# Kernel optimization log

Hardware: AMD Instinct MI355X
Metric: run time of the kernel (lower is better)

Reference implementation:

```python
import jax, jax.numpy as jnp
import numpy as np

B, S, D = 2, 2048, 1024
H, DK = 16, 64            # n_heads, d_k = d_model // n_heads
EXP = 4                   # pattern-separation expand_factor
ED = DK * EXP             # expanded_dim = 256
TOPK = 32                 # top-k kept after ReLU expansion
ALPHA = 0.05
TNT = 1.0                 # trace_norm_target


def setup_inputs() -> dict:
    key = jax.random.key(0)
    ks = jax.random.split(key, 8)
    sc = 1.0 / np.sqrt(D)
    x = jax.random.normal(ks[0], (B, S, D), jnp.float32)
    W_q = jax.random.normal(ks[1], (D, D), jnp.float32) * sc
    W_k = jax.random.normal(ks[2], (D, D), jnp.float32) * sc
    W_v = jax.random.normal(ks[3], (D, D), jnp.float32) * sc
    W_o = jax.random.normal(ks[4], (D, D), jnp.float32) * sc
    # trace buffers (non-zero so the trace read path actually matters)
    traces = jax.random.normal(ks[5], (H, DK, DK), jnp.float32) * 0.02
    value_traces = jax.random.normal(ks[6], (H, ED, DK), jnp.float32) * 0.02
    # frozen random expansion projection (dentate gyrus), W / sqrt(d_k)
    W_expand = jax.random.normal(ks[7], (DK, ED), jnp.float32) / np.sqrt(DK)
    return dict(x=x, W_q=W_q, W_k=W_k, W_v=W_v, W_o=W_o,
                traces=traces, value_traces=value_traces, W_expand=W_expand)


def _eff_alpha(T):
    # alpha / (1 + ||T_h||_F / trace_norm_target), shape (1, H, 1, 1)
    norms = jnp.sqrt(jnp.sum(T * T, axis=(1, 2)))
    return (ALPHA / (1.0 + norms / TNT)).reshape(1, -1, 1, 1)


def _forward(x, W_q, W_k, W_v, W_o, traces, value_traces, W_expand):
    b, s, d = x.shape
    def proj(W):
        return jnp.einsum('bsd,de->bse', x, W).reshape(b, s, H, DK).transpose(0, 2, 1, 3)
    Q, K, V = proj(W_q), proj(W_k), proj(W_v)  # (B, H, S, DK)

    scores = jnp.einsum('bhqd,bhkd->bhqk', Q, K)
    # score trace bias: alpha_eff * (Q @ T @ K^T)
    QT = jnp.einsum('bhqd,hde->bhqe', Q, traces)
    trace_scores = jnp.einsum('bhqe,bhke->bhqk', QT, K)
    scores = (scores + _eff_alpha(traces) * trace_scores) / np.sqrt(DK)
    A = jax.nn.softmax(scores, axis=-1)
    out = jnp.einsum('bhqk,bhkd->bhqd', A, V)

    # value trace read with use_key_q shift: address with previous token's Q
    Q_addr = jnp.concatenate([jnp.zeros_like(Q[:, :, :1, :]), Q[:, :, :-1, :]], axis=2)
    # pattern separation: frozen random expansion + ReLU + top-k sparsify
    Q_exp = jax.nn.relu(jnp.einsum('bhsd,de->bhse', Q_addr, W_expand))  # (B,H,S,ED)
    kth = jax.lax.top_k(Q_exp, TOPK)[0][..., -1:]
    Q_sparse = jnp.where(Q_exp >= kth, Q_exp, 0.0)  # == scatter of top-k vals (ties at 0 contribute 0)
    stored = jnp.einsum('bhse,hed->bhsd', Q_sparse, value_traces)
    out = out + _eff_alpha(value_traces) * stored

    out = out.transpose(0, 2, 1, 3).reshape(b, s, d)
    return jnp.einsum('bsd,de->bse', out, W_o)


def reference(x, W_q, W_k, W_v, W_o, traces, value_traces, W_expand):
    return _forward(x, W_q, W_k, W_v, W_o, traces, value_traces, W_expand)
```

## Files before the change

### kernel.cpp

```cpp
#include <hip/hip_runtime.h>
#include <stdint.h>

#define Bn 2
#define Sn 2048
#define Dn 1024
#define Hn 16
#define DKn 64
#define EDn 256

typedef __attribute__((ext_vector_type(8))) short bvec8;
typedef __attribute__((ext_vector_type(4))) float fvec4;

#define MFMA(a, b, c) __builtin_amdgcn_mfma_f32_16x16x32_bf16(a, b, c, 0, 0, 0)

__device__ __forceinline__ float b2f(unsigned short u) {
  return __uint_as_float(((unsigned)u) << 16);
}
__device__ __forceinline__ unsigned short f2b(float x) {
  unsigned u = __float_as_uint(x);
  u += 0x7fffu + ((u >> 16) & 1u);
  return (unsigned short)(u >> 16);
}
__device__ __forceinline__ unsigned pk2(float a, float b) {
  return ((__float_as_uint(a) + 0x8000u) >> 16) |
         ((__float_as_uint(b) + 0x8000u) & 0xffff0000u);
}
__device__ __forceinline__ void g2l(const unsigned short* g, unsigned short* l) {
  __builtin_amdgcn_global_load_lds(
      (const __attribute__((address_space(1))) void*)g,
      (__attribute__((address_space(3))) void*)l, 16, 0, 0);
}

__global__ __launch_bounds__(256) void k_prep1(
    const float* __restrict__ x, const float* __restrict__ w0,
    const float* __restrict__ w1, const float* __restrict__ w2,
    const float* __restrict__ w3, const float* __restrict__ traces,
    const float* __restrict__ vtr, const float* __restrict__ Wexp,
    unsigned short* __restrict__ Wt, unsigned short* __restrict__ WexpT,
    unsigned short* __restrict__ xb, float* __restrict__ alphas,
    unsigned short* __restrict__ VTt) {
  const int blk = blockIdx.x;
  const int tid = threadIdx.x;
  __shared__ unsigned short Tl[64][72];
  if (blk < 1024) {
    int z = blk >> 8, t = blk & 255;
    int n0 = (t & 15) * 64, k0 = (t >> 4) * 64;
    const float* src = (z == 0) ? w0 : ((z == 1) ? w1 : ((z == 2) ? w2 : w3));
    unsigned short* d = Wt + (size_t)z * Dn * Dn;
#pragma unroll
    for (int i = 0; i < 4; ++i) {
      int q = tid + 256 * i;
      int kr = q >> 4, c4 = q & 15;
      float4 v = *(const float4*)&src[(size_t)(k0 + kr) * Dn + n0 + 4 * c4];
      ushort4 u;
      u.x = f2b(v.x); u.y = f2b(v.y); u.z = f2b(v.z); u.w = f2b(v.w);
      *(ushort4*)&Tl[kr][4 * c4] = u;
    }
    __syncthreads();
#pragma unroll
    for (int i = 0; i < 4; ++i) {
      int q = tid + 256 * i;
      int nr = q >> 4, c4 = q & 15;
      ushort4 u;
      u.x = Tl[4 * c4 + 0][nr]; u.y = Tl[4 * c4 + 1][nr];
      u.z = Tl[4 * c4 + 2][nr]; u.w = Tl[4 * c4 + 3][nr];
      *(ushort4*)&d[(size_t)(n0 + nr) * Dn + k0 + 4 * c4] = u;
    }
  } else if (blk < 1028) {
    int e0 = (blk - 1024) * 64;
#pragma unroll
    for (int i = 0; i < 4; ++i) {
      int q = tid + 256 * i;
      int dr = q >> 4, c4 = q & 15;
      float4 v = *(const float4*)&Wexp[(size_t)dr * EDn + e0 + 4 * c4];
      ushort4 u;
      u.x = f2b(v.x); u.y = f2b(v.y); u.z = f2b(v.z); u.w = f2b(v.w);
      *(ushort4*)&Tl[dr][4 * c4] = u;
    }
    __syncthreads();
#pragma unroll
    for (int i = 0; i < 4; ++i) {
      int q = tid + 256 * i;
      int er = q >> 4, c4 = q & 15;
      ushort4 u;
      u.x = Tl[4 * c4 + 0][er]; u.y = Tl[4 * c4 + 1][er];
      u.z = Tl[4 * c4 + 2][er]; u.w = Tl[4 * c4 + 3][er];
      *(ushort4*)&WexpT[(size_t)(e0 + er) * DKn + 4 * c4] = u;
    }
  } else if (blk < 5124) {
    size_t i = ((size_t)(blk - 1028) * 256 + tid) * 4;
    float4 v = *(const float4*)&x[i];
    ushort4 u;
    u.x = f2b(v.x); u.y = f2b(v.y); u.z = f2b(v.z); u.w = f2b(v.w);
    *(ushort4*)&xb[i] = u;
  } else if (blk < 5156) {
    int a = blk - 5124;
    const float* base;
    int n;
    if (a < 16) { base = traces + a * DKn * DKn; n = DKn * DKn; }
    else        { base = vtr + (a - 16) * EDn * DKn; n = EDn * DKn; }
    float s = 0.f;
    for (int i = tid; i < n; i += 256) { float v = base[i]; s += v * v; }
    __shared__ float red[256];
    red[tid] = s;
    __syncthreads();
    for (int off = 128; off > 0; off >>= 1) {
      if (tid < off) red[tid] += red[tid + off];
      __syncthreads();
    }
    if (tid == 0) alphas[a] = 0.05f / (1.f + sqrtf(red[0]));
  } else {
    int t = blk - 5156;
    int e0 = (t & 3) * 64, h = t >> 2;
    const float* src = vtr + (size_t)h * EDn * DKn;
    unsigned short* dst = VTt + (size_t)h * DKn * EDn;
#pragma unroll
    for (int i = 0; i < 4; ++i) {
      int q = tid + 256 * i;
      int er = q >> 4, c4 = q & 15;
      float4 v = *(const float4*)&src[(size_t)(e0 + er) * DKn + 4 * c4];
      ushort4 u;
      u.x = f2b(v.x); u.y = f2b(v.y); u.z = f2b(v.z); u.w = f2b(v.w);
      *(ushort4*)&Tl[er][4 * c4] = u;
    }
    __syncthreads();
#pragma unroll
    for (int i = 0; i < 4; ++i) {
      int q = tid + 256 * i;
      int dr = q >> 4, c4 = q & 15;
      ushort4 u;
      u.x = Tl[4 * c4 + 0][dr]; u.y = Tl[4 * c4 + 1][dr];
      u.z = Tl[4 * c4 + 2][dr]; u.w = Tl[4 * c4 + 3][dr];
      *(ushort4*)&dst[(size_t)dr * EDn + e0 + 4 * c4] = u;
    }
  }
}

__global__ __launch_bounds__(256) void k_mkM(const float* __restrict__ tr,
                                             const float* __restrict__ alph,
                                             unsigned short* __restrict__ Mt) {
  const float SC = 0.125f * 1.4426950408889634f;
  int h = blockIdx.x;
  float a = alph[h] * SC;
  const float* th = tr + (size_t)h * DKn * DKn;
  unsigned short* mh = Mt + (size_t)h * DKn * DKn;
  for (int i = threadIdx.x; i < DKn * DKn; i += 256) {
    int e = i >> 6, k = i & 63;
    float v = a * th[(size_t)k * DKn + e] + ((e == k) ? SC : 0.f);
    mh[i] = f2b(v);
  }
}

template <int MODE>
__global__ __launch_bounds__(256) void k_gemm(
    const unsigned short* __restrict__ Ab,
    const unsigned short* __restrict__ BtBase, unsigned short* __restrict__ Qb,
    unsigned short* __restrict__ Kb, unsigned short* __restrict__ VtOut,
    float* __restrict__ Cout) {
  const int z = (MODE == 0) ? blockIdx.z : 0;
  const unsigned short* Bt = BtBase + (size_t)z * Dn * Dn;
  __shared__ unsigned short As[128 * 32];
  __shared__ unsigned short Bs[128 * 32];
  const int tid = threadIdx.x;
  const int w = tid >> 6, lane = tid & 63, qd = lane >> 4, cc = lane & 15;
  const int m0 = blockIdx.y * 128, n0 = blockIdx.x * 128;
  const int mW = 64 * (w >> 1), nW = 64 * (w & 1);
  const int srow = lane >> 2;
  const int schk = 8 * ((lane & 3) ^ (srow & 3));
  const int r0 = 32 * w + srow, r1 = r0 + 16;
  const bool swap = (MODE == 1) || (z != 2);
  fvec4 acc[4][4];
#pragma unroll
  for (int i = 0; i < 4; ++i)
#pragma unroll
    for (int j = 0; j < 4; ++j) acc[i][j] = (fvec4){0.f, 0.f, 0.f, 0.f};

  for (int k0 = 0; k0 < Dn; k0 += 32) {
    g2l(&Ab[(size_t)(m0 + r0) * Dn + k0 + schk], &As[1024 * w]);
    g2l(&Ab[(size_t)(m0 + r1) * Dn + k0 + schk], &As[1024 * w + 512]);
    g2l(&Bt[(size_t)(n0 + r0) * Dn + k0 + schk], &Bs[1024 * w]);
    g2l(&Bt[(size_t)(n0 + r1) * Dn + k0 + schk], &Bs[1024 * w + 512]);
    __syncthreads();
    bvec8 af[4], bf[4];
#pragma unroll
    for (int i = 0; i < 4; ++i) {
      int ra = mW + 16 * i + cc;
      af[i] = *(const bvec8*)&As[ra * 32 + 8 * (qd ^ (ra & 3))];
      int rb = nW + 16 * i + cc;
      bf[i] = *(const bvec8*)&Bs[rb * 32 + 8 * (qd ^ (rb & 3))];
    }
    if (swap) {
#pragma unroll
      for (int i = 0; i < 4; ++i)
#pragma unroll
        for (int j = 0; j < 4; ++j) acc[i][j] = MFMA(bf[j], af[i], acc[i][j]);
    } else {
#pragma unroll
      for (int i = 0; i < 4; ++i)
#pragma unroll
        for (int j = 0; j < 4; ++j) acc[i][j] = MFMA(af[i], bf[j], acc[i][j]);
    }
    __syncthreads();
  }
#pragma unroll
  for (int i = 0; i < 4; ++i)
#pragma unroll
    for (int j = 0; j < 4; ++j) {
      if (MODE == 1) {
        int s = m0 + mW + 16 * i + cc;
        int nb = n0 + nW + 16 * j + 4 * qd;
        float4 v = make_float4(acc[i][j][0], acc[i][j][1], acc[i][j][2],
                               acc[i][j][3]);
        *(float4*)&Cout[(size_t)s * Dn + nb] = v;
      } else if (z == 2) {
        int rowb = m0 + mW + 16 * i + 4 * qd;
        int col = n0 + nW + 16 * j + cc;
        int b = rowb >> 11, s = rowb & 2047;
        int h = col >> 6, dk = col & 63;
        ushort4 u;
        u.x = f2b(acc[i][j][0]); u.y = f2b(acc[i][j][1]);
        u.z = f2b(acc[i][j][2]); u.w = f2b(acc[i][j][3]);
        *(ushort4*)&VtOut[(((size_t)(b * Hn + h)) * DKn + dk) * Sn + s] = u;
      } else {
        int s = m0 + mW + 16 * i + cc;
        int col = n0 + nW + 16 * j + 4 * qd;
        int b = s >> 11;
        int sm = s & 2047;
        int h = col >> 6, dk = col & 63;
        unsigned short* Cb = (z == 0) ? Qb : Kb;
        ushort4 u;
        u.x = f2b(acc[i][j][0]); u.y = f2b(acc[i][j][1]);
        u.z = f2b(acc[i][j][2]); u.w = f2b(acc[i][j][3]);
        *(ushort4*)&Cb[(((size_t)(b * Hn + h)) * Sn + sm) * DKn + dk] = u;
      }
    }
}

__global__ __launch_bounds__(256, 2) void k_pattsep(
    const unsigned short* __restrict__ Qb,
    const unsigned short* __restrict__ WexpT,
    const unsigned short* __restrict__ VTt,
    const float* __restrict__ alphas, unsigned short* __restrict__ ATb) {
  __shared__ uint4 Wl4[2048];
  __shared__ uint4 Vl4[2048];
  __shared__ uint4 Ps4[4][256];
  const int tile = blockIdx.x, bh = blockIdx.y;
  const int b = bh >> 4, h = bh & 15;
  const int tid = threadIdx.x;
  const int w = tid >> 6, lane = tid & 63, qd = lane >> 4, cc = lane & 15;
  const float avt = alphas[16 + h];

  const uint4* wsrc = (const uint4*)WexpT;
  const uint4* vsrc = (const uint4*)(VTt + (size_t)h * DKn * EDn);
  for (int i = tid; i < 2048; i += 256) {
    int e = i >> 3, c = i & 7;
    Wl4[e * 8 + (c ^ (e & 7))] = wsrc[i];
    int d = i >> 5, c2 = i & 31;
    Vl4[d * 32 + (c2 ^ (d & 7))] = vsrc[i];
  }
  __syncthreads();

  const unsigned short* Wls = (const unsigned short*)Wl4;
  const unsigned short* Vls = (const unsigned short*)Vl4;
  unsigned short* Pw = (unsigned short*)Ps4[w];

  for (int rg = 0; rg < 2; ++rg) {
    const int s0 = tile * 128 + w * 32 + rg * 16;
    bvec8 aq0 = {}, aq1 = {};
    const int srow = s0 + cc;
    if (srow > 0) {
      const unsigned short* qp = Qb + ((size_t)bh * Sn + srow - 1) * DKn;
      aq0 = *(const bvec8*)&qp[8 * qd];
      aq1 = *(const bvec8*)&qp[32 + 8 * qd];
    }
    fvec4 E[16];
#pragma unroll
    for (int j = 0; j < 16; ++j) {
      const int e = 16 * j + cc;
      const unsigned short* wr = Wls + e * 64;
      bvec8 b0 = *(const bvec8*)&wr[8 * (qd ^ (e & 7))];
      bvec8 b1 = *(const bvec8*)&wr[8 * ((4 + qd) ^ (e & 7))];
      fvec4 zv = {0.f, 0.f, 0.f, 0.f};
      zv = MFMA(aq0, b0, zv);
      E[j] = MFMA(aq1, b1, zv);
    }
#pragma unroll
    for (int j = 0; j < 16; ++j)
#pragma unroll
      for (int r = 0; r < 4; ++r) E[j][r] = fmaxf(E[j][r], 0.f);

    float thr[4];
#pragma unroll
    for (int r = 0; r < 4; ++r) {
      unsigned cur = 0u;
      bool done = false;
      for (int bit = 30; bit >= 0; --bit) {
        unsigned cand = cur | (1u << bit);
        float t = __uint_as_float(cand);
        int cnt = 0;
#pragma unroll
        for (int j = 0; j < 16; ++j) cnt += (E[j][r] >= t) ? 1 : 0;
        cnt += __shfl_xor(cnt, 1);
        cnt += __shfl_xor(cnt, 2);
        cnt += __shfl_xor(cnt, 4);
        cnt += __shfl_xor(cnt, 8);
        if (!done && cnt >= 32) {
          cur = cand;
          if (cnt == 32) done = true;
        }
        if (__all(done)) break;
      }
      thr[r] = __uint_as_float(cur);
    }

    fvec4 acc2[4];
#pragma unroll
    for (int j2 = 0; j2 < 4; ++j2) acc2[j2] = (fvec4){0.f, 0.f, 0.f, 0.f};

#pragma unroll
    for (int half = 0; half < 2; ++half) {
#pragma unroll
      for (int j = 0; j < 8; ++j) {
        const int jj = j + 8 * half;
#pragma unroll
        for (int r = 0; r < 4; ++r) {
          float v = E[jj][r];
          bool sel = (v >= thr[r]) && (v > 0.f);
          int row = 4 * qd + r;
          int s = 16 * j + cc;
          int ch = (s >> 3) ^ (row & 7);
          Pw[row * 128 + ch * 8 + (s & 7)] = sel ? f2b(v) : (unsigned short)0;
        }
      }
#pragma unroll
      for (int j2 = 0; j2 < 4; ++j2) {
        const int d = 16 * j2 + cc;
        const unsigned short* vr = Vls + d * 256;
#pragma unroll
        for (int c = 0; c < 4; ++c) {
          int cg = 4 * (c + 4 * half) + qd;
          bvec8 bv = *(const bvec8*)&vr[8 * (cg ^ (d & 7))];
          int ca = 4 * c + qd;
          bvec8 ap = *(const bvec8*)&Pw[cc * 128 + 8 * (ca ^ (cc & 7))];
          acc2[j2] = MFMA(ap, bv, acc2[j2]);
        }
      }
    }
#pragma unroll
    for (int j2 = 0; j2 < 4; ++j2)
#pragma unroll
      for (int r = 0; r < 4; ++r) {
        int row = s0 + 4 * qd + r;
        ATb[((size_t)(b * Sn + row)) * Dn + h * DKn + 16 * j2 + cc] =
            f2b(avt * acc2[j2][r]);
      }
  }
}

__global__ __launch_bounds__(256) void k_attn(
    const unsigned short* __restrict__ Qb, const unsigned short* __restrict__ Kb,
    const unsigned short* __restrict__ Vt, const unsigned short* __restrict__ Mt,
    unsigned short* __restrict__ ATb) {
  __shared__ unsigned short Kd[64 * 64];
  __shared__ unsigned short Vl[64 * 64];
  __shared__ unsigned short Ps[4][16][72];
  const int bh = blockIdx.x, qt = blockIdx.y;
  const int b = bh >> 4, h = bh & 15;
  const int tid = threadIdx.x;
  const int w = tid >> 6, lane = tid & 63, qd = lane >> 4, cc = lane & 15;

  const unsigned short* qg = Qb + ((size_t)bh * Sn + qt * 64 + w * 16) * DKn;
  bvec8 a0 = *(const bvec8*)&qg[cc * DKn + 8 * qd];
  bvec8 a1 = *(const bvec8*)&qg[cc * DKn + 32 + 8 * qd];
  const unsigned short* mh = Mt + (size_t)h * DKn * DKn;
#pragma unroll
  for (int j = 0; j < 4; ++j) {
    bvec8 b0 = *(const bvec8*)&mh[(size_t)(16 * j + cc) * DKn + 8 * qd];
    bvec8 b1 = *(const bvec8*)&mh[(size_t)(16 * j + cc) * DKn + 32 + 8 * qd];
    fvec4 zz = {0.f, 0.f, 0.f, 0.f};
    zz = MFMA(a0, b0, zz);
    zz = MFMA(a1, b1, zz);
#pragma unroll
    for (int r = 0; r < 4; ++r) {
      int qr = 4 * qd + r;
      Kd[(16 * w + qr) * 64 + 8 * ((2 * j + (cc >> 3)) ^ (qr & 7)) + (cc & 7)] =
          f2b(zz[r]);
    }
  }
  bvec8 aq0 = *(const bvec8*)&Kd[(16 * w + cc) * 64 + 8 * (qd ^ (cc & 7))];
  bvec8 aq1 =
      *(const bvec8*)&Kd[(16 * w + cc) * 64 + 8 * ((qd + 4) ^ (cc & 7))];

  float l_s = 0.f;
  fvec4 O[4];
#pragma unroll
  for (int j = 0; j < 4; ++j) O[j] = (fvec4){0.f, 0.f, 0.f, 0.f};

  const int vrow = lane >> 3;
  const int vchk = 8 * ((lane & 7) ^ (vrow & 7));
  const unsigned short* kgb = Kb + (size_t)bh * Sn * DKn;
  const unsigned short* vgb = Vt + (size_t)bh * DKn * Sn;

  for (int kt = 0; kt < Sn / 64; ++kt) {
    __syncthreads();
    const unsigned short* kg = kgb + (size_t)kt * 64 * DKn;
    g2l(&kg[(size_t)(16 * w + vrow) * 64 + vchk], &Kd[1024 * w]);
    g2l(&kg[(size_t)(16 * w + 8 + vrow) * 64 + vchk], &Kd[1024 * w + 512]);
    g2l(&vgb[(size_t)(16 * w + vrow) * Sn + kt * 64 + vchk], &Vl[1024 * w]);
    g2l(&vgb[(size_t)(16 * w + 8 + vrow) * Sn + kt * 64 + vchk],
        &Vl[1024 * w + 512]);
    __syncthreads();
    fvec4 sc[4];
#pragma unroll
    for (int j = 0; j < 4; ++j) {
      int rk = 16 * j + cc;
      bvec8 b0 = *(const bvec8*)&Kd[rk * 64 + 8 * (qd ^ (cc & 7))];
      bvec8 b1 = *(const bvec8*)&Kd[rk * 64 + 8 * ((qd + 4) ^ (cc & 7))];
      fvec4 zz = {0.f, 0.f, 0.f, 0.f};
      zz = MFMA(b0, aq0, zz);
      sc[j] = MFMA(b1, aq1, zz);
    }
#pragma unroll
    for (int j = 0; j < 4; ++j) {
      float p0 = __builtin_amdgcn_exp2f(sc[j][0]);
      float p1 = __builtin_amdgcn_exp2f(sc[j][1]);
      float p2 = __builtin_amdgcn_exp2f(sc[j][2]);
      float p3 = __builtin_amdgcn_exp2f(sc[j][3]);
      l_s += (p0 + p1) + (p2 + p3);
      uint2 u;
      u.x = pk2(p0, p1);
      u.y = pk2(p2, p3);
      *(uint2*)&Ps[w][cc][16 * j + 4 * qd] = u;
    }
    bvec8 ap0 = *(const bvec8*)&Ps[w][cc][8 * qd];
    bvec8 ap1 = *(const bvec8*)&Ps[w][cc][32 + 8 * qd];
#pragma unroll
    for (int j = 0; j < 4; ++j) {
      int rv = 16 * j + cc;
      bvec8 v0 = *(const bvec8*)&Vl[rv * 64 + 8 * (qd ^ (cc & 7))];
      bvec8 v1 = *(const bvec8*)&Vl[rv * 64 + 8 * ((qd + 4) ^ (cc & 7))];
      O[j] = MFMA(ap0, v0, O[j]);
      O[j] = MFMA(ap1, v1, O[j]);
    }
  }
  l_s += __shfl_xor(l_s, 16);
  l_s += __shfl_xor(l_s, 32);
  float linv = 1.f / l_s;
  float inv[4];
#pragma unroll
  for (int r = 0; r < 4; ++r) inv[r] = __shfl(linv, 4 * qd + r);
#pragma unroll
  for (int j = 0; j < 4; ++j)
#pragma unroll
    for (int r = 0; r < 4; ++r) {
      int row = qt * 64 + w * 16 + 4 * qd + r;
      unsigned short* p =
          ATb + ((size_t)(b * Sn + row)) * Dn + h * DKn + 16 * j + cc;
      *p = f2b(b2f(*p) + O[j][r] * inv[r]);
    }
}

extern "C" void kernel_launch(void* const* d_in, const int* in_sizes, int n_in,
                              void* d_out, int out_size, void* d_ws,
                              size_t ws_size, hipStream_t stream) {
  const float* x = (const float*)d_in[0];
  const float* Wq = (const float*)d_in[1];
  const float* Wk = (const float*)d_in[2];
  const float* Wv = (const float*)d_in[3];
  const float* Wo = (const float*)d_in[4];
  const float* traces = (const float*)d_in[5];
  const float* vtr = (const float*)d_in[6];
  const float* Wexp = (const float*)d_in[7];

  const size_t NQ = (size_t)Bn * Hn * Sn * DKn;
  unsigned short* Qb = (unsigned short*)d_ws;
  unsigned short* Kb = Qb + NQ;
  unsigned short* Vt = Kb + NQ;
  unsigned short* Wt = Vt + NQ;
  unsigned short* Mt = Wt + NQ;
  unsigned short* WexpT = Mt + 65536;
  unsigned short* VTt = WexpT + 16384;
  float* alph = (float*)(VTt + 262144);
  unsigned short* ATb = (unsigned short*)(alph + 32);
  unsigned short* xb = ATb;

  k_prep1<<<5220, 256, 0, stream>>>(x, Wq, Wk, Wv, Wo, traces, vtr, Wexp, Wt,
                                    WexpT, xb, alph, VTt);
  k_mkM<<<16, 256, 0, stream>>>(traces, alph, Mt);
  k_gemm<0><<<dim3(8, 32, 3), 256, 0, stream>>>(xb, Wt, Qb, Kb, Vt, nullptr);
  k_pattsep<<<dim3(16, 32), 256, 0, stream>>>(Qb, WexpT, VTt, alph, ATb);
  k_attn<<<dim3(32, 32), 256, 0, stream>>>(Qb, Kb, Vt, Mt, ATb);
  k_gemm<1><<<dim3(8, 32, 1), 256, 0, stream>>>(
      ATb, Wt + 3 * (size_t)Dn * Dn, nullptr, nullptr, nullptr,
      (float*)d_out);
}
```

Before: 315.4 us.

## Process two key tiles per barrier in attention and fold M build into prep

The attention loop now stages 128 keys and values per iteration in two LDS buffers. This halves the number of block-wide barriers and gives more global-to-LDS loads in flight per sync. The P scratch uses an XOR-swizzled 64-wide layout to reduce bank conflicts. Separately, the trace-norm and M-matrix construction move into the prep kernel, removing one launch and its serial dependency. The trade-off is a larger LDS footprint per attention block, which may lower how many blocks fit per CU.

```diff
diff --git a/kernel.cpp b/kernel.cpp
--- a/kernel.cpp
+++ b/kernel.cpp
@@ -31,19 +31,102 @@
       (__attribute__((address_space(3))) void*)l, 16, 0, 0);
 }
 
-__global__ __launch_bounds__(256) void k_prep1(
+__global__ __launch_bounds__(256) void k_prep(
     const float* __restrict__ x, const float* __restrict__ w0,
     const float* __restrict__ w1, const float* __restrict__ w2,
     const float* __restrict__ w3, const float* __restrict__ traces,
     const float* __restrict__ vtr, const float* __restrict__ Wexp,
     unsigned short* __restrict__ Wt, unsigned short* __restrict__ WexpT,
     unsigned short* __restrict__ xb, float* __restrict__ alphas,
-    unsigned short* __restrict__ VTt) {
+    unsigned short* __restrict__ VTt, unsigned short* __restrict__ Mt) {
   const int blk = blockIdx.x;
   const int tid = threadIdx.x;
   __shared__ unsigned short Tl[64][72];
-  if (blk < 1024) {
-    int z = blk >> 8, t = blk & 255;
+  __shared__ float red[256];
+  if (blk < 16) {
+    const float* base = vtr + (size_t)blk * EDn * DKn;
+    float s = 0.f;
+    for (int i = tid; i < EDn * DKn; i += 256) { float v = base[i]; s += v * v; }
+    red[tid] = s;
+    __syncthreads();
+    for (int off = 128; off > 0; off >>= 1) {
+      if (tid < off) red[tid] += red[tid + off];
+      __syncthreads();
+    }
+    if (tid == 0) alphas[16 + blk] = 0.05f / (1.f + sqrtf(red[0]));
+  } else if (blk < 32) {
+    __shared__ float Ts[DKn * DKn];
+    const float SC = 0.125f * 1.4426950408889634f;
+    int h = blk - 16;
+    const float* th = traces + (size_t)h * DKn * DKn;
+    float s = 0.f;
+    for (int i = tid; i < DKn * DKn; i += 256) {
+      float v = th[i];
+      Ts[i] = v;
+      s += v * v;
+    }
+    red[tid] = s;
+    __syncthreads();
+    for (int off = 128; off > 0; off >>= 1) {
+      if (tid < off) red[tid] += red[tid + off];
+      __syncthreads();
+    }
+    float a = (0.05f / (1.f + sqrtf(red[0]))) * SC;
+    unsigned short* mh = Mt + (size_t)h * DKn * DKn;
+    for (int i = tid; i < DKn * DKn; i += 256) {
+      int e = i >> 6, k = i & 63;
+      float v = a * Ts[k * DKn + e] + ((e == k) ? SC : 0.f);
+      mh[i] = f2b(v);
+    }
+  } else if (blk < 96) {
+    int t = blk - 32;
+    int e0 = (t & 3) * 64, h = t >> 2;
+    const float* src = vtr + (size_t)h * EDn * DKn;
+    unsigned short* dst = VTt + (size_t)h * DKn * EDn;
+#pragma unroll
+    for (int i = 0; i < 4; ++i) {
+      int q = tid + 256 * i;
+      int er = q >> 4, c4 = q & 15;
+      float4 v = *(const float4*)&src[(size_t)(e0 + er) * DKn + 4 * c4];
+      ushort4 u;
+      u.x = f2b(v.x); u.y = f2b(v.y); u.z = f2b(v.z); u.w = f2b(v.w);
+      *(ushort4*)&Tl[er][4 * c4] = u;
+    }
+    __syncthreads();
+#pragma unroll
+    for (int i = 0; i < 4; ++i) {
+      int q = tid + 256 * i;
+      int dr = q >> 4, c4 = q & 15;
+      ushort4 u;
+      u.x = Tl[4 * c4 + 0][dr]; u.y = Tl[4 * c4 + 1][dr];
+      u.z = Tl[4 * c4 + 2][dr]; u.w = Tl[4 * c4 + 3][dr];
+      *(ushort4*)&dst[(size_t)dr * EDn + e0 + 4 * c4] = u;
+    }
+  } else if (blk < 100) {
+    int e0 = (blk - 96) * 64;
+#pragma unroll
+    for (int i = 0; i < 4; ++i) {
+      int q = tid + 256 * i;
+      int dr = q >> 4, c4 = q & 15;
+      float4 v = *(const float4*)&Wexp[(size_t)dr * EDn + e0 + 4 * c4];
+      ushort4 u;
+      u.x = f2b(v.x); u.y = f2b(v.y); u.z = f2b(v.z); u.w = f2b(v.w);
+      *(ushort4*)&Tl[dr][4 * c4] = u;
+    }
+    __syncthreads();
+#pragma unroll
+    for (int i = 0; i < 4; ++i) {
+      int q = tid + 256 * i;
+      int er = q >> 4, c4 = q & 15;
+      ushort4 u;
+      u.x = Tl[4 * c4 + 0][er]; u.y = Tl[4 * c4 + 1][er];
+      u.z = Tl[4 * c4 + 2][er]; u.w = Tl[4 * c4 + 3][er];
+      *(ushort4*)&WexpT[(size_t)(e0 + er) * DKn + 4 * c4] = u;
+    }
+  } else if (blk < 1124) {
+    int t = blk - 100;
+    int z = t >> 8;
+    t &= 255;
     int n0 = (t & 15) * 64, k0 = (t >> 4) * 64;
     const float* src = (z == 0) ? w0 : ((z == 1) ? w1 : ((z == 2) ? w2 : w3));
     unsigned short* d = Wt + (size_t)z * Dn * Dn;
@@ -66,88 +149,12 @@
       u.z = Tl[4 * c4 + 2][nr]; u.w = Tl[4 * c4 + 3][nr];
       *(ushort4*)&d[(size_t)(n0 + nr) * Dn + k0 + 4 * c4] = u;
     }
-  } else if (blk < 1028) {
-    int e0 = (blk - 1024) * 64;
-#pragma unroll
-    for (int i = 0; i < 4; ++i) {
-      int q = tid + 256 * i;
-      int dr = q >> 4, c4 = q & 15;
-      float4 v = *(const float4*)&Wexp[(size_t)dr * EDn + e0 + 4 * c4];
-      ushort4 u;
-      u.x = f2b(v.x); u.y = f2b(v.y); u.z = f2b(v.z); u.w = f2b(v.w);
-      *(ushort4*)&Tl[dr][4 * c4] = u;
-    }
-    __syncthreads();
-#pragma unroll
-    for (int i = 0; i < 4; ++i) {
-      int q = tid + 256 * i;
-      int er = q >> 4, c4 = q & 15;
-      ushort4 u;
-      u.x = Tl[4 * c4 + 0][er]; u.y = Tl[4 * c4 + 1][er];
-      u.z = Tl[4 * c4 + 2][er]; u.w = Tl[4 * c4 + 3][er];
-      *(ushort4*)&WexpT[(size_t)(e0 + er) * DKn + 4 * c4] = u;
-    }
-  } else if (blk < 5124) {
-    size_t i = ((size_t)(blk - 1028) * 256 + tid) * 4;
+  } else {
+    size_t i = ((size_t)(blk - 1124) * 256 + tid) * 4;
     float4 v = *(const float4*)&x[i];
     ushort4 u;
     u.x = f2b(v.x); u.y = f2b(v.y); u.z = f2b(v.z); u.w = f2b(v.w);
     *(ushort4*)&xb[i] = u;
-  } else if (blk < 5156) {
-    int a = blk - 5124;
-    const float* base;
-    int n;
-    if (a < 16) { base = traces + a * DKn * DKn; n = DKn * DKn; }
-    else        { base = vtr + (a - 16) * EDn * DKn; n = EDn * DKn; }
-    float s = 0.f;
-    for (int i = tid; i < n; i += 256) { float v = base[i]; s += v * v; }
-    __shared__ float red[256];
-    red[tid] = s;
-    __syncthreads();
-    for (int off = 128; off > 0; off >>= 1) {
-      if (tid < off) red[tid] += red[tid + off];
-      __syncthreads();
-    }
-    if (tid == 0) alphas[a] = 0.05f / (1.f + sqrtf(red[0]));
-  } else {
-    int t = blk - 5156;
-    int e0 = (t & 3) * 64, h = t >> 2;
-    const float* src = vtr + (size_t)h * EDn * DKn;
-    unsigned short* dst = VTt + (size_t)h * DKn * EDn;
-#pragma unroll
-    for (int i = 0; i < 4; ++i) {
-      int q = tid + 256 * i;
-      int er = q >> 4, c4 = q & 15;
-      float4 v = *(const float4*)&src[(size_t)(e0 + er) * DKn + 4 * c4];
-      ushort4 u;
-      u.x = f2b(v.x); u.y = f2b(v.y); u.z = f2b(v.z); u.w = f2b(v.w);
-      *(ushort4*)&Tl[er][4 * c4] = u;
-    }
-    __syncthreads();
-#pragma unroll
-    for (int i = 0; i < 4; ++i) {
-      int q = tid + 256 * i;
-      int dr = q >> 4, c4 = q & 15;
-      ushort4 u;
-      u.x = Tl[4 * c4 + 0][dr]; u.y = Tl[4 * c4 + 1][dr];
-      u.z = Tl[4 * c4 + 2][dr]; u.w = Tl[4 * c4 + 3][dr];
-      *(ushort4*)&dst[(size_t)dr * EDn + e0 + 4 * c4] = u;
-    }
-  }
-}
-
-__global__ __launch_bounds__(256) void k_mkM(const float* __restrict__ tr,
-                                             const float* __restrict__ alph,
-                                             unsigned short* __restrict__ Mt) {
-  const float SC = 0.125f * 1.4426950408889634f;
-  int h = blockIdx.x;
-  float a = alph[h] * SC;
-  const float* th = tr + (size_t)h * DKn * DKn;
-  unsigned short* mh = Mt + (size_t)h * DKn * DKn;
-  for (int i = threadIdx.x; i < DKn * DKn; i += 256) {
-    int e = i >> 6, k = i & 63;
-    float v = a * th[(size_t)k * DKn + e] + ((e == k) ? SC : 0.f);
-    mh[i] = f2b(v);
   }
 }
 
@@ -361,9 +368,9 @@
     const unsigned short* __restrict__ Qb, const unsigned short* __restrict__ Kb,
     const unsigned short* __restrict__ Vt, const unsigned short* __restrict__ Mt,
     unsigned short* __restrict__ ATb) {
-  __shared__ unsigned short Kd[64 * 64];
-  __shared__ unsigned short Vl[64 * 64];
-  __shared__ unsigned short Ps[4][16][72];
+  __shared__ unsigned short Kd2[2][4096];
+  __shared__ unsigned short Vl2[2][4096];
+  __shared__ unsigned short Ps[4][2048];
   const int bh = blockIdx.x, qt = blockIdx.y;
   const int b = bh >> 4, h = bh & 15;
   const int tid = threadIdx.x;
@@ -383,13 +390,13 @@
 #pragma unroll
     for (int r = 0; r < 4; ++r) {
       int qr = 4 * qd + r;
-      Kd[(16 * w + qr) * 64 + 8 * ((2 * j + (cc >> 3)) ^ (qr & 7)) + (cc & 7)] =
-          f2b(zz[r]);
+      Kd2[0][(16 * w + qr) * 64 + 8 * ((2 * j + (cc >> 3)) ^ (qr & 7)) +
+             (cc & 7)] = f2b(zz[r]);
     }
   }
-  bvec8 aq0 = *(const bvec8*)&Kd[(16 * w + cc) * 64 + 8 * (qd ^ (cc & 7))];
+  bvec8 aq0 = *(const bvec8*)&Kd2[0][(16 * w + cc) * 64 + 8 * (qd ^ (cc & 7))];
   bvec8 aq1 =
-      *(const bvec8*)&Kd[(16 * w + cc) * 64 + 8 * ((qd + 4) ^ (cc & 7))];
+      *(const bvec8*)&Kd2[0][(16 * w + cc) * 64 + 8 * ((qd + 4) ^ (cc & 7))];
 
   float l_s = 0.f;
   fvec4 O[4];
@@ -400,47 +407,61 @@
   const int vchk = 8 * ((lane & 7) ^ (vrow & 7));
   const unsigned short* kgb = Kb + (size_t)bh * Sn * DKn;
   const unsigned short* vgb = Vt + (size_t)bh * DKn * Sn;
-
-  for (int kt = 0; kt < Sn / 64; ++kt) {
-    __syncthreads();
-    const unsigned short* kg = kgb + (size_t)kt * 64 * DKn;
-    g2l(&kg[(size_t)(16 * w + vrow) * 64 + vchk], &Kd[1024 * w]);
-    g2l(&kg[(size_t)(16 * w + 8 + vrow) * 64 + vchk], &Kd[1024 * w + 512]);
-    g2l(&vgb[(size_t)(16 * w + vrow) * Sn + kt * 64 + vchk], &Vl[1024 * w]);
-    g2l(&vgb[(size_t)(16 * w + 8 + vrow) * Sn + kt * 64 + vchk],
-        &Vl[1024 * w + 512]);
-    __syncthreads();
-    fvec4 sc[4];
-#pragma unroll
-    for (int j = 0; j < 4; ++j) {
-      int rk = 16 * j + cc;
-      bvec8 b0 = *(const bvec8*)&Kd[rk * 64 + 8 * (qd ^ (cc & 7))];
-      bvec8 b1 = *(const bvec8*)&Kd[rk * 64 + 8 * ((qd + 4) ^ (cc & 7))];
-      fvec4 zz = {0.f, 0.f, 0.f, 0.f};
-      zz = MFMA(b0, aq0, zz);
-      sc[j] = MFMA(b1, aq1, zz);
-    }
-#pragma unroll
-    for (int j = 0; j < 4; ++j) {
-      float p0 = __builtin_amdgcn_exp2f(sc[j][0]);
-      float p1 = __builtin_amdgcn_exp2f(sc[j][1]);
-      float p2 = __builtin_amdgcn_exp2f(sc[j][2]);
-      float p3 = __builtin_amdgcn_exp2f(sc[j][3]);
-      l_s += (p0 + p1) + (p2 + p3);
-      uint2 u;
-      u.x = pk2(p0, p1);
-      u.y = pk2(p2, p3);
-      *(uint2*)&Ps[w][cc][16 * j + 4 * qd] = u;
-    }
-    bvec8 ap0 = *(const bvec8*)&Ps[w][cc][8 * qd];
-    bvec8 ap1 = *(const bvec8*)&Ps[w][cc][32 + 8 * qd];
-#pragma unroll
-    for (int j = 0; j < 4; ++j) {
-      int rv = 16 * j + cc;
-      bvec8 v0 = *(const bvec8*)&Vl[rv * 64 + 8 * (qd ^ (cc & 7))];
-      bvec8 v1 = *(const bvec8*)&Vl[rv * 64 + 8 * ((qd + 4) ^ (cc & 7))];
-      O[j] = MFMA(ap0, v0, O[j]);
-      O[j] = MFMA(ap1, v1, O[j]);
+  unsigned short* Pw = Ps[w];
+
+  for (int kt2 = 0; kt2 < Sn / 128; ++kt2) {
+    __syncthreads();
+    const unsigned short* kg = kgb + (size_t)kt2 * 128 * DKn;
+    const int c0 = kt2 * 128;
+    g2l(&kg[(size_t)(16 * w + vrow) * 64 + vchk], &Kd2[0][1024 * w]);
+    g2l(&kg[(size_t)(16 * w + 8 + vrow) * 64 + vchk], &Kd2[0][1024 * w + 512]);
+    g2l(&kg[(size_t)(64 + 16 * w + vrow) * 64 + vchk], &Kd2[1][1024 * w]);
+    g2l(&kg[(size_t)(64 + 16 * w + 8 + vrow) * 64 + vchk],
+        &Kd2[1][1024 * w + 512]);
+    g2l(&vgb[(size_t)(16 * w + vrow) * Sn + c0 + vchk], &Vl2[0][1024 * w]);
+    g2l(&vgb[(size_t)(16 * w + 8 + vrow) * Sn + c0 + vchk],
+        &Vl2[0][1024 * w + 512]);
+    g2l(&vgb[(size_t)(16 * w + vrow) * Sn + c0 + 64 + vchk], &Vl2[1][1024 * w]);
+    g2l(&vgb[(size_t)(16 * w + 8 + vrow) * Sn + c0 + 64 + vchk],
+        &Vl2[1][1024 * w + 512]);
+    __syncthreads();
+#pragma unroll
+    for (int t = 0; t < 2; ++t) {
+      const unsigned short* Kd = Kd2[t];
+      const unsigned short* Vl = Vl2[t];
+      fvec4 sc[4];
+#pragma unroll
+      for (int j = 0; j < 4; ++j) {
+        int rk = 16 * j + cc;
+        bvec8 b0 = *(const bvec8*)&Kd[rk * 64 + 8 * (qd ^ (cc & 7))];
+        bvec8 b1 = *(const bvec8*)&Kd[rk * 64 + 8 * ((qd + 4) ^ (cc & 7))];
+        fvec4 zz = {0.f, 0.f, 0.f, 0.f};
+        zz = MFMA(b0, aq0, zz);
+        sc[j] = MFMA(b1, aq1, zz);
+      }
+#pragma unroll
+      for (int j = 0; j < 4; ++j) {
+        float p0 = __builtin_amdgcn_exp2f(sc[j][0]);
+        float p1 = __builtin_amdgcn_exp2f(sc[j][1]);
+        float p2 = __builtin_amdgcn_exp2f(sc[j][2]);
+        float p3 = __builtin_amdgcn_exp2f(sc[j][3]);
+        l_s += (p0 + p1) + (p2 + p3);
+        uint2 u;
+        u.x = pk2(p0, p1);
+        u.y = pk2(p2, p3);
+        *(uint2*)&Pw[cc * 64 + 8 * ((2 * j + (qd >> 1)) ^ (cc & 7)) +
+                     4 * (qd & 1)] = u;
+      }
+      bvec8 ap0 = *(const bvec8*)&Pw[cc * 64 + 8 * (qd ^ (cc & 7))];
+      bvec8 ap1 = *(const bvec8*)&Pw[cc * 64 + 8 * ((qd + 4) ^ (cc & 7))];
+#pragma unroll
+      for (int j = 0; j < 4; ++j) {
+        int rv = 16 * j + cc;
+        bvec8 v0 = *(const bvec8*)&Vl[rv * 64 + 8 * (qd ^ (cc & 7))];
+        bvec8 v1 = *(const bvec8*)&Vl[rv * 64 + 8 * ((qd + 4) ^ (cc & 7))];
+        O[j] = MFMA(ap0, v0, O[j]);
+        O[j] = MFMA(ap1, v1, O[j]);
+      }
     }
   }
   l_s += __shfl_xor(l_s, 16);
@@ -484,9 +505,8 @@
   unsigned short* ATb = (unsigned short*)(alph + 32);
   unsigned short* xb = ATb;
 
-  k_prep1<<<5220, 256, 0, stream>>>(x, Wq, Wk, Wv, Wo, traces, vtr, Wexp, Wt,
-                                    WexpT, xb, alph, VTt);
-  k_mkM<<<16, 256, 0, stream>>>(traces, alph, Mt);
+  k_prep<<<5220, 256, 0, stream>>>(x, Wq, Wk, Wv, Wo, traces, vtr, Wexp, Wt,
+                                   WexpT, xb, alph, VTt, Mt);
   k_gemm<0><<<dim3(8, 32, 3), 256, 0, stream>>>(xb, Wt, Qb, Kb, Vt, nullptr);
   k_pattsep<<<dim3(16, 32), 256, 0, stream>>>(Qb, WexpT, VTt, alph, ATb);
   k_attn<<<dim3(32, 32), 256, 0, stream>>>(Qb, Kb, Vt, Mt, ATb);
```

Measured after the change: 315.5 us. No clear change (+0.0%).
